# Optimization experiments

Hardware: AMD Instinct MI355X
Metric: run time of the kernel (lower is better)

Reference implementation:

```python
import jax, jax.numpy as jnp
import numpy as np

N_NODES = 10000
N_EDGES = 160000
F_DIM = 64
H = 4


def setup_inputs() -> dict:
    key = jax.random.key(0)
    ks = jax.random.split(key, 10)
    s = 1.0 / np.sqrt(F_DIM)  # xavier-ish scale
    return {
        "x": jax.random.normal(ks[0], (N_NODES, F_DIM), jnp.float32),
        "edge_index": jax.random.randint(ks[1], (2, N_EDGES), 0, N_NODES),
        "edge_vec": jax.random.normal(ks[2], (N_EDGES, 3), jnp.float32),
        "edge_len": jax.random.uniform(ks[3], (N_EDGES,), jnp.float32, 0.1, 5.0),
        "w_proj_W": jax.random.normal(ks[4], (H, F_DIM, F_DIM), jnp.float32) * s,
        "radial_W": jax.random.normal(ks[5], (H, F_DIM, F_DIM), jnp.float32) * s,
        "tangential_W": jax.random.normal(ks[6], (H, F_DIM, F_DIM), jnp.float32) * s,
        "radial_score": jax.random.normal(ks[7], (H, F_DIM), jnp.float32) * s,
        "tangential_score": jax.random.normal(ks[8], (H, F_DIM), jnp.float32) * s,
        "radial_distance_log_scale": jnp.zeros((), jnp.float32),
        "radial_temp_bias": jnp.zeros((H,), jnp.float32),
        "radial_temp_weight": jnp.zeros((H,), jnp.float32),
        "w_out_W": jax.random.normal(ks[9], (F_DIM, F_DIM), jnp.float32) * s,
    }


def _segment_softmax(logits, receiver, num_nodes):
    # logits: [E, H]; softmax over all edges sharing the same receiver.
    # Equivalent to the original's degree-bucketed per-group softmax.
    m = jax.ops.segment_max(logits, receiver, num_segments=num_nodes)  # [N, H]
    a = jnp.exp(logits - m[receiver])
    d = jax.ops.segment_sum(a, receiver, num_segments=num_nodes)       # [N, H]
    return a / d[receiver]


def reference(x, edge_index, edge_vec, edge_len, w_proj_W, radial_W, tangential_W,
              radial_score, tangential_score, radial_distance_log_scale,
              radial_temp_bias, radial_temp_weight, w_out_W):
    sender, receiver = edge_index[0], edge_index[1]
    n = x.shape[0]

    # Per-head bias-free linear projections (o3.Linear on scalar irreps).
    energy = jnp.einsum('nf,hfg->hng', x, w_proj_W)       # [H, N, F]
    radial = jnp.einsum('nf,hfg->hng', x, radial_W)       # [H, N, F]
    tang = jnp.einsum('nf,hfg->hng', x, tangential_W)     # [H, N, F]

    e_d = energy[:, sender] - energy[:, receiver]                       # [H, E, F]
    r_d = jnp.transpose(radial[:, sender] - radial[:, receiver], (1, 0, 2))  # [E, H, F]
    t_d = jnp.transpose(tang[:, sender] - tang[:, receiver], (1, 0, 2))      # [E, H, F]

    scale = jax.nn.softplus(radial_distance_log_scale)
    r_log = jnp.einsum('hef,hf->eh', e_d, radial_score) - scale * edge_len[:, None]  # [E, H]
    temp = jax.nn.softplus(radial_temp_bias[None, :] + radial_temp_weight[None, :] * edge_len[:, None])
    r_log = r_log / (temp + 0.0001)
    t_log = jnp.einsum('hef,hf->eh', e_d, tangential_score)                          # [E, H]

    r_alpha = _segment_softmax(r_log, receiver, n)  # [E, H]
    t_alpha = _segment_softmax(t_log, receiver, n)  # [E, H]

    r_msg = jax.ops.segment_sum(r_alpha[:, :, None] * r_d, receiver, num_segments=n)  # [N, H, F]
    t_msg = jax.ops.segment_sum(t_alpha[:, :, None] * t_d, receiver, num_segments=n)  # [N, H, F]

    out = jnp.nan_to_num((r_msg + t_msg).mean(axis=1))  # mean over heads -> [N, F]
    return x + out @ w_out_W
```

## Files before the change

kernel.cpp:

```cpp
#include <hip/hip_runtime.h>
#include <math.h>

#define N_NODES 10000
#define N_EDGES 160000
#define CAP 64

#define NB_SCORE 40
#define NB_BUCKET 625
#define NB_WPP 9
#define NB_D1 (NB_SCORE + NB_BUCKET + NB_WPP)

typedef short bf16x8 __attribute__((ext_vector_type(8)));
typedef float f32x4 __attribute__((ext_vector_type(4)));

__device__ __forceinline__ float bf2f(unsigned short u) {
    return __uint_as_float(((unsigned int)u) << 16);
}
__device__ __forceinline__ unsigned short f2bf(float f) {
    unsigned int x = __float_as_uint(f);
    unsigned int r = (x + 0x7fffu + ((x >> 16) & 1u)) >> 16;
    return (unsigned short)r;
}
__device__ __forceinline__ float softplus_f(float x) {
    return fmaxf(x, 0.f) + log1pf(expf(-fabsf(x)));
}

__global__ void __launch_bounds__(256) k_prep(const float* __restrict__ x,
                                              const float* __restrict__ wproj,
                                              const float* __restrict__ wrad,
                                              const float* __restrict__ wtan,
                                              const float* __restrict__ rsc,
                                              const float* __restrict__ tsc,
                                              const float* __restrict__ wout,
                                              const int* __restrict__ ei,
                                              const float* __restrict__ el,
                                              float* __restrict__ rs,
                                              float* __restrict__ ts,
                                              int* __restrict__ cur,
                                              int2* __restrict__ sbuf,
                                              unsigned short* __restrict__ wppT) {
    __shared__ __align__(16) float smem[8192];
    int b = blockIdx.x;
    int t = threadIdx.x;

    if (b < NB_SCORE) {
        float* vrl = smem;
        float* vtl = smem + 256;
        {
            int h = t >> 6, f = t & 63;
            const float* wrow = wproj + h * 4096 + f * 64;
            const float* rsp = rsc + h * 64;
            const float* tsp = tsc + h * 64;
            float ar = 0.f, at = 0.f;
            for (int g = 0; g < 64; ++g) {
                float w = wrow[g];
                ar += w * rsp[g];
                at += w * tsp[g];
            }
            vrl[t] = ar;
            vtl[t] = at;
        }
        __syncthreads();
        int n = b * 256 + t;
        if (n >= N_NODES) return;
        const float4* xr = (const float4*)(x + n * 64);
        float accr[4] = {0.f, 0.f, 0.f, 0.f};
        float acct[4] = {0.f, 0.f, 0.f, 0.f};
        for (int i = 0; i < 16; ++i) {
            float4 xv = xr[i];
#pragma unroll
            for (int h = 0; h < 4; ++h) {
                float4 a = ((const float4*)vrl)[h * 16 + i];
                accr[h] += xv.x * a.x + xv.y * a.y + xv.z * a.z + xv.w * a.w;
                float4 bb = ((const float4*)vtl)[h * 16 + i];
                acct[h] += xv.x * bb.x + xv.y * bb.y + xv.z * bb.z + xv.w * bb.w;
            }
        }
        ((float4*)rs)[n] = make_float4(accr[0], accr[1], accr[2], accr[3]);
        ((float4*)ts)[n] = make_float4(acct[0], acct[1], acct[2], acct[3]);
    } else if (b < NB_SCORE + NB_BUCKET) {
        int e = (b - NB_SCORE) * 256 + t;
        if (e >= N_EDGES) return;
        int s = ei[e];
        int r = ei[N_EDGES + e];
        float len = el[e];
        int pos = atomicAdd(&cur[r], 1);
        if (pos < CAP) sbuf[r * CAP + pos] = make_int2(s, __float_as_int(len));
    } else {
        int k = b - NB_SCORE - NB_BUCKET;
        float* wo = smem;
        float* am = smem + 4096;
        for (int i = 0; i < 16; ++i) wo[t + 256 * i] = wout[t + 256 * i];
        if (k < 8) {
            const float* M = (k < 4) ? (wrad + k * 4096) : (wtan + (k - 4) * 4096);
            for (int i = 0; i < 16; ++i) am[t + 256 * i] = M[t + 256 * i];
        } else {
            for (int i = 0; i < 16; ++i) {
                int e = t + 256 * i;
                float s = 0.f;
#pragma unroll
                for (int h = 0; h < 4; ++h) s += wrad[h * 4096 + e] + wtan[h * 4096 + e];
                am[e] = -s;
            }
        }
        __syncthreads();
        int c = t & 63;
        int fg = t >> 6;
        for (int j = 0; j < 16; ++j) {
            int f = fg * 16 + j;
            float acc = 0.f;
            for (int g = 0; g < 64; ++g) acc += am[f * 64 + g] * wo[g * 64 + c];
            wppT[c * 576 + k * 64 + f] = f2bf(acc * 0.25f);
        }
    }
}

__global__ void __launch_bounds__(1024, 8) k_node(const int* __restrict__ cur,
                                                  const int2* __restrict__ sbuf,
                                                  const float* __restrict__ rs,
                                                  const float* __restrict__ ts,
                                                  const float* __restrict__ rdls,
                                                  const float* __restrict__ tb,
                                                  const float* __restrict__ tw,
                                                  const float* __restrict__ x,
                                                  const unsigned short* __restrict__ wppT,
                                                  float* __restrict__ out) {
    __shared__ __align__(16) unsigned short accL[16 * 584];
    __shared__ __align__(16) float aldsb[16][CAP * 8];
    __shared__ int sldsb[16][CAP];
    int t = threadIdx.x;
    int wid = t >> 6, lane = t & 63;
    int blk = blockIdx.x;

    float scale = softplus_f(rdls[0]);
    float tb0 = tb[0], tb1 = tb[1], tb2 = tb[2], tb3 = tb[3];
    float tw0 = tw[0], tw1 = tw[1], tw2 = tw[2], tw3 = tw[3];
    float* alds = aldsb[wid];
    int*   slds = sldsb[wid];

    int n = blk * 16 + wid;
    int deg = min(cur[n], CAP);

    float4 rsr = ((const float4*)rs)[n];
    float4 tsr = ((const float4*)ts)[n];

    const float NEG = -3.402823466e38f;
    float rl0 = NEG, rl1 = NEG, rl2 = NEG, rl3 = NEG;
    float tl0 = NEG, tl1 = NEG, tl2 = NEG, tl3 = NEG;
    int s_e = 0;
    if (lane < deg) {
        int2 sl = sbuf[n * CAP + lane];
        s_e = sl.x;
        float len = __int_as_float(sl.y);
        float4 rss = ((const float4*)rs)[s_e];
        float4 tss = ((const float4*)ts)[s_e];
        float sl0 = scale * len;
        float i0 = 1.f / (softplus_f(tb0 + tw0 * len) + 1e-4f);
        float i1 = 1.f / (softplus_f(tb1 + tw1 * len) + 1e-4f);
        float i2 = 1.f / (softplus_f(tb2 + tw2 * len) + 1e-4f);
        float i3 = 1.f / (softplus_f(tb3 + tw3 * len) + 1e-4f);
        rl0 = ((rss.x - rsr.x) - sl0) * i0;
        rl1 = ((rss.y - rsr.y) - sl0) * i1;
        rl2 = ((rss.z - rsr.z) - sl0) * i2;
        rl3 = ((rss.w - rsr.w) - sl0) * i3;
        tl0 = tss.x - tsr.x;
        tl1 = tss.y - tsr.y;
        tl2 = tss.z - tsr.z;
        tl3 = tss.w - tsr.w;
    }
    float mr0 = rl0, mr1 = rl1, mr2 = rl2, mr3 = rl3;
    float mt0 = tl0, mt1 = tl1, mt2 = tl2, mt3 = tl3;
#pragma unroll
    for (int d = 32; d >= 1; d >>= 1) {
        mr0 = fmaxf(mr0, __shfl_xor(mr0, d)); mr1 = fmaxf(mr1, __shfl_xor(mr1, d));
        mr2 = fmaxf(mr2, __shfl_xor(mr2, d)); mr3 = fmaxf(mr3, __shfl_xor(mr3, d));
        mt0 = fmaxf(mt0, __shfl_xor(mt0, d)); mt1 = fmaxf(mt1, __shfl_xor(mt1, d));
        mt2 = fmaxf(mt2, __shfl_xor(mt2, d)); mt3 = fmaxf(mt3, __shfl_xor(mt3, d));
    }
    float er0 = 0.f, er1 = 0.f, er2 = 0.f, er3 = 0.f;
    float et0 = 0.f, et1 = 0.f, et2 = 0.f, et3 = 0.f;
    if (lane < deg) {
        er0 = expf(rl0 - mr0); er1 = expf(rl1 - mr1);
        er2 = expf(rl2 - mr2); er3 = expf(rl3 - mr3);
        et0 = expf(tl0 - mt0); et1 = expf(tl1 - mt1);
        et2 = expf(tl2 - mt2); et3 = expf(tl3 - mt3);
    }
    float sr0 = er0, sr1 = er1, sr2 = er2, sr3 = er3;
    float st0 = et0, st1 = et1, st2 = et2, st3 = et3;
#pragma unroll
    for (int d = 32; d >= 1; d >>= 1) {
        sr0 += __shfl_xor(sr0, d); sr1 += __shfl_xor(sr1, d);
        sr2 += __shfl_xor(sr2, d); sr3 += __shfl_xor(sr3, d);
        st0 += __shfl_xor(st0, d); st1 += __shfl_xor(st1, d);
        st2 += __shfl_xor(st2, d); st3 += __shfl_xor(st3, d);
    }
    if (lane < deg) {
        float* ap = alds + lane * 8;
        ((float4*)ap)[0] = make_float4(er0 / sr0, er1 / sr1, er2 / sr2, er3 / sr3);
        ((float4*)ap)[1] = make_float4(et0 / st0, et1 / st1, et2 / st2, et3 / st3);
        slds[lane] = s_e;
    }

    float a0 = 0.f, a1 = 0.f, a2 = 0.f, a3 = 0.f;
    float b0 = 0.f, b1 = 0.f, b2 = 0.f, b3 = 0.f;
    int i = 0;
    for (; i + 4 <= deg; i += 4) {
        int s0 = slds[i], s1 = slds[i + 1], s2 = slds[i + 2], s3 = slds[i + 3];
        float xv0 = x[s0 * 64 + lane];
        float xv1 = x[s1 * 64 + lane];
        float xv2 = x[s2 * 64 + lane];
        float xv3 = x[s3 * 64 + lane];
        float4 ar0 = ((const float4*)(alds + i * 8))[0];
        float4 at0 = ((const float4*)(alds + i * 8))[1];
        float4 ar1 = ((const float4*)(alds + (i + 1) * 8))[0];
        float4 at1 = ((const float4*)(alds + (i + 1) * 8))[1];
        float4 ar2 = ((const float4*)(alds + (i + 2) * 8))[0];
        float4 at2 = ((const float4*)(alds + (i + 2) * 8))[1];
        float4 ar3 = ((const float4*)(alds + (i + 3) * 8))[0];
        float4 at3 = ((const float4*)(alds + (i + 3) * 8))[1];
        a0 += ar0.x * xv0 + ar1.x * xv1 + ar2.x * xv2 + ar3.x * xv3;
        a1 += ar0.y * xv0 + ar1.y * xv1 + ar2.y * xv2 + ar3.y * xv3;
        a2 += ar0.z * xv0 + ar1.z * xv1 + ar2.z * xv2 + ar3.z * xv3;
        a3 += ar0.w * xv0 + ar1.w * xv1 + ar2.w * xv2 + ar3.w * xv3;
        b0 += at0.x * xv0 + at1.x * xv1 + at2.x * xv2 + at3.x * xv3;
        b1 += at0.y * xv0 + at1.y * xv1 + at2.y * xv2 + at3.y * xv3;
        b2 += at0.z * xv0 + at1.z * xv1 + at2.z * xv2 + at3.z * xv3;
        b3 += at0.w * xv0 + at1.w * xv1 + at2.w * xv2 + at3.w * xv3;
    }
    for (; i < deg; ++i) {
        int s0 = slds[i];
        float xv0 = x[s0 * 64 + lane];
        float4 ar0 = ((const float4*)(alds + i * 8))[0];
        float4 at0 = ((const float4*)(alds + i * 8))[1];
        a0 += ar0.x * xv0; a1 += ar0.y * xv0; a2 += ar0.z * xv0; a3 += ar0.w * xv0;
        b0 += at0.x * xv0; b1 += at0.y * xv0; b2 += at0.z * xv0; b3 += at0.w * xv0;
    }
    float c8 = (deg > 0) ? x[n * 64 + lane] : 0.f;

    unsigned short* arow = accL + wid * 584;
    arow[0 * 64 + lane] = f2bf(a0);
    arow[1 * 64 + lane] = f2bf(a1);
    arow[2 * 64 + lane] = f2bf(a2);
    arow[3 * 64 + lane] = f2bf(a3);
    arow[4 * 64 + lane] = f2bf(b0);
    arow[5 * 64 + lane] = f2bf(b1);
    arow[6 * 64 + lane] = f2bf(b2);
    arow[7 * 64 + lane] = f2bf(b3);
    arow[8 * 64 + lane] = f2bf(c8);
    __syncthreads();

    if (wid < 4) {
        int c = lane & 15, q = lane >> 4;
        f32x4 dacc = {0.f, 0.f, 0.f, 0.f};
        const unsigned short* bp = wppT + (16 * wid + c) * 576 + q * 8;
        const unsigned short* ap = accL + c * 584 + q * 8;
#pragma unroll
        for (int kc = 0; kc < 18; ++kc) {
            bf16x8 af = *(const bf16x8*)(ap + kc * 32);
            bf16x8 bf = *(const bf16x8*)(bp + kc * 32);
            dacc = __builtin_amdgcn_mfma_f32_16x16x32_bf16(af, bf, dacc, 0, 0, 0);
        }
#pragma unroll
        for (int r = 0; r < 4; ++r) {
            int node = blk * 16 + q * 4 + r;
            int col = 16 * wid + c;
            out[node * 64 + col] = x[node * 64 + col] + dacc[r];
        }
    }
}

extern "C" void kernel_launch(void* const* d_in, const int* in_sizes, int n_in,
                              void* d_out, int out_size, void* d_ws, size_t ws_size,
                              hipStream_t stream) {
    const float* x     = (const float*)d_in[0];
    const int*   ei    = (const int*)d_in[1];
    const float* el    = (const float*)d_in[3];
    const float* wproj = (const float*)d_in[4];
    const float* wrad  = (const float*)d_in[5];
    const float* wtan  = (const float*)d_in[6];
    const float* rsc   = (const float*)d_in[7];
    const float* tsc   = (const float*)d_in[8];
    const float* rdls  = (const float*)d_in[9];
    const float* tb    = (const float*)d_in[10];
    const float* tw    = (const float*)d_in[11];
    const float* wout  = (const float*)d_in[12];
    float* out = (float*)d_out;

    char* w = (char*)d_ws;
    size_t o = 0;
    auto nxt = [&](size_t bytes) -> char* {
        char* p = w + o;
        o += (bytes + 255) & ~(size_t)255;
        return p;
    };
    float* rs = (float*)nxt((size_t)N_NODES * 4 * 4);
    float* ts = (float*)nxt((size_t)N_NODES * 4 * 4);
    int*   cur = (int*)nxt((size_t)N_NODES * 4);
    int2*  sbuf = (int2*)nxt((size_t)N_NODES * CAP * 8);
    unsigned short* wppT = (unsigned short*)nxt((size_t)64 * 576 * 2);

    hipMemsetAsync(cur, 0, (size_t)N_NODES * 4, stream);

    k_prep<<<NB_D1, 256, 0, stream>>>(x, wproj, wrad, wtan, rsc, tsc, wout,
                                      ei, el, rs, ts, cur, sbuf, wppT);
    k_node<<<625, 1024, 0, stream>>>(cur, sbuf, rs, ts, rdls, tb, tw, x, wppT, out);
}
```

Baseline: 127.1 us.

## Fuse memset, prep and node kernels into one persistent kernel with grid barriers

Replaces the memset plus two kernel launches with a single persistent kernel of 512 blocks that zeroes the counters, runs the prep tasks (scores, edge bucketing, weight prefold) on a subset of blocks, and then processes node tiles in a grid-stride loop. A software sense-reversing grid barrier separates the phases, removing launch overhead and inter-kernel gaps. It also interleaves the radial and tangential score arrays into one buffer and switches expf to __expf. The risk is that the grid barrier assumes all 512 blocks of 1024 threads are co-resident; if they are not, the kernel deadlocks. Phase imbalance also means blocks may idle at the barrier.

Measured after the change: 229.7 us. 1.81x slower.

```diff
diff --git a/kernel.cpp b/kernel.cpp
--- a/kernel.cpp
+++ b/kernel.cpp
@@ -4,11 +4,7 @@
 #define N_NODES 10000
 #define N_EDGES 160000
 #define CAP 64
-
-#define NB_SCORE 40
-#define NB_BUCKET 625
-#define NB_WPP 9
-#define NB_D1 (NB_SCORE + NB_BUCKET + NB_WPP)
+#define GRID 512
 
 typedef short bf16x8 __attribute__((ext_vector_type(8)));
 typedef float f32x4 __attribute__((ext_vector_type(4)));
@@ -22,249 +18,277 @@
     return (unsigned short)r;
 }
 __device__ __forceinline__ float softplus_f(float x) {
-    return fmaxf(x, 0.f) + log1pf(expf(-fabsf(x)));
-}
-
-__global__ void __launch_bounds__(256) k_prep(const float* __restrict__ x,
-                                              const float* __restrict__ wproj,
-                                              const float* __restrict__ wrad,
-                                              const float* __restrict__ wtan,
-                                              const float* __restrict__ rsc,
-                                              const float* __restrict__ tsc,
-                                              const float* __restrict__ wout,
-                                              const int* __restrict__ ei,
-                                              const float* __restrict__ el,
-                                              float* __restrict__ rs,
-                                              float* __restrict__ ts,
-                                              int* __restrict__ cur,
-                                              int2* __restrict__ sbuf,
-                                              unsigned short* __restrict__ wppT) {
-    __shared__ __align__(16) float smem[8192];
+    return fmaxf(x, 0.f) + log1pf(__expf(-fabsf(x)));
+}
+
+__device__ unsigned int g_cnt = 0;
+__device__ unsigned int g_sense = 0;
+
+__device__ __forceinline__ void gbar() {
+    __syncthreads();
+    if (threadIdx.x == 0) {
+        unsigned int e = __hip_atomic_load(&g_sense, __ATOMIC_RELAXED, __HIP_MEMORY_SCOPE_AGENT);
+        unsigned int old = __hip_atomic_fetch_add(&g_cnt, 1, __ATOMIC_RELEASE, __HIP_MEMORY_SCOPE_AGENT);
+        if (old == GRID - 1) {
+            __hip_atomic_store(&g_cnt, 0, __ATOMIC_RELAXED, __HIP_MEMORY_SCOPE_AGENT);
+            __hip_atomic_fetch_add(&g_sense, 1, __ATOMIC_RELEASE, __HIP_MEMORY_SCOPE_AGENT);
+        } else {
+            while (__hip_atomic_load(&g_sense, __ATOMIC_RELAXED, __HIP_MEMORY_SCOPE_AGENT) == e)
+                __builtin_amdgcn_s_sleep(2);
+        }
+        __builtin_amdgcn_fence(__ATOMIC_ACQUIRE, "agent");
+    }
+    __syncthreads();
+}
+
+__global__ void __launch_bounds__(1024, 8) k_fused(const float* __restrict__ x,
+                                                   const int* __restrict__ ei,
+                                                   const float* __restrict__ el,
+                                                   const float* __restrict__ wproj,
+                                                   const float* __restrict__ wrad,
+                                                   const float* __restrict__ wtan,
+                                                   const float* __restrict__ rsc,
+                                                   const float* __restrict__ tsc,
+                                                   const float* __restrict__ rdls,
+                                                   const float* __restrict__ tb,
+                                                   const float* __restrict__ tw,
+                                                   const float* __restrict__ wout,
+                                                   float* __restrict__ rts,
+                                                   int* __restrict__ cur,
+                                                   int2* __restrict__ sbuf,
+                                                   unsigned short* __restrict__ wppT,
+                                                   float* __restrict__ out) {
+    __shared__ __align__(16) char smem[55552];
     int b = blockIdx.x;
     int t = threadIdx.x;
-
-    if (b < NB_SCORE) {
-        float* vrl = smem;
-        float* vtl = smem + 256;
-        {
-            int h = t >> 6, f = t & 63;
-            const float* wrow = wproj + h * 4096 + f * 64;
-            const float* rsp = rsc + h * 64;
-            const float* tsp = tsc + h * 64;
-            float ar = 0.f, at = 0.f;
-            for (int g = 0; g < 64; ++g) {
-                float w = wrow[g];
-                ar += w * rsp[g];
-                at += w * tsp[g];
-            }
-            vrl[t] = ar;
-            vtl[t] = at;
-        }
-        __syncthreads();
-        int n = b * 256 + t;
-        if (n >= N_NODES) return;
-        const float4* xr = (const float4*)(x + n * 64);
-        float accr[4] = {0.f, 0.f, 0.f, 0.f};
-        float acct[4] = {0.f, 0.f, 0.f, 0.f};
-        for (int i = 0; i < 16; ++i) {
-            float4 xv = xr[i];
-#pragma unroll
-            for (int h = 0; h < 4; ++h) {
-                float4 a = ((const float4*)vrl)[h * 16 + i];
-                accr[h] += xv.x * a.x + xv.y * a.y + xv.z * a.z + xv.w * a.w;
-                float4 bb = ((const float4*)vtl)[h * 16 + i];
-                acct[h] += xv.x * bb.x + xv.y * bb.y + xv.z * bb.z + xv.w * bb.w;
-            }
-        }
-        ((float4*)rs)[n] = make_float4(accr[0], accr[1], accr[2], accr[3]);
-        ((float4*)ts)[n] = make_float4(acct[0], acct[1], acct[2], acct[3]);
-    } else if (b < NB_SCORE + NB_BUCKET) {
-        int e = (b - NB_SCORE) * 256 + t;
-        if (e >= N_EDGES) return;
-        int s = ei[e];
-        int r = ei[N_EDGES + e];
-        float len = el[e];
-        int pos = atomicAdd(&cur[r], 1);
-        if (pos < CAP) sbuf[r * CAP + pos] = make_int2(s, __float_as_int(len));
-    } else {
-        int k = b - NB_SCORE - NB_BUCKET;
-        float* wo = smem;
-        float* am = smem + 4096;
-        for (int i = 0; i < 16; ++i) wo[t + 256 * i] = wout[t + 256 * i];
-        if (k < 8) {
-            const float* M = (k < 4) ? (wrad + k * 4096) : (wtan + (k - 4) * 4096);
-            for (int i = 0; i < 16; ++i) am[t + 256 * i] = M[t + 256 * i];
+    int wid = t >> 6, lane = t & 63;
+
+    {
+        int idx = b * 1024 + t;
+        if (idx < N_NODES) cur[idx] = 0;
+    }
+    gbar();
+
+    if (b >= 336) {
+        int task = 511 - b;
+        if (task < 10) {
+            float* vrl = (float*)smem;
+            float* vtl = vrl + 256;
+            if (t < 256) {
+                int h = t >> 6, f = t & 63;
+                const float* wrow = wproj + h * 4096 + f * 64;
+                const float* rsp = rsc + h * 64;
+                const float* tsp = tsc + h * 64;
+                float ar = 0.f, at = 0.f;
+                for (int g = 0; g < 64; ++g) {
+                    float w = wrow[g];
+                    ar += w * rsp[g];
+                    at += w * tsp[g];
+                }
+                vrl[t] = ar;
+                vtl[t] = at;
+            }
+            __syncthreads();
+            int n = task * 1024 + t;
+            if (n < N_NODES) {
+                const float4* xr = (const float4*)(x + n * 64);
+                float accr[4] = {0.f, 0.f, 0.f, 0.f};
+                float acct[4] = {0.f, 0.f, 0.f, 0.f};
+                for (int i = 0; i < 16; ++i) {
+                    float4 xv = xr[i];
+#pragma unroll
+                    for (int h = 0; h < 4; ++h) {
+                        float4 a = ((const float4*)vrl)[h * 16 + i];
+                        accr[h] += xv.x * a.x + xv.y * a.y + xv.z * a.z + xv.w * a.w;
+                        float4 bb = ((const float4*)vtl)[h * 16 + i];
+                        acct[h] += xv.x * bb.x + xv.y * bb.y + xv.z * bb.z + xv.w * bb.w;
+                    }
+                }
+                ((float4*)rts)[n * 2]     = make_float4(accr[0], accr[1], accr[2], accr[3]);
+                ((float4*)rts)[n * 2 + 1] = make_float4(acct[0], acct[1], acct[2], acct[3]);
+            }
+        } else if (task < 167) {
+            int e = (task - 10) * 1024 + t;
+            if (e < N_EDGES) {
+                int s = ei[e];
+                int r = ei[N_EDGES + e];
+                float len = el[e];
+                int pos = atomicAdd(&cur[r], 1);
+                if (pos < CAP) sbuf[r * CAP + pos] = make_int2(s, __float_as_int(len));
+            }
         } else {
-            for (int i = 0; i < 16; ++i) {
-                int e = t + 256 * i;
-                float s = 0.f;
-#pragma unroll
-                for (int h = 0; h < 4; ++h) s += wrad[h * 4096 + e] + wtan[h * 4096 + e];
-                am[e] = -s;
-            }
-        }
-        __syncthreads();
-        int c = t & 63;
-        int fg = t >> 6;
-        for (int j = 0; j < 16; ++j) {
-            int f = fg * 16 + j;
-            float acc = 0.f;
-            for (int g = 0; g < 64; ++g) acc += am[f * 64 + g] * wo[g * 64 + c];
-            wppT[c * 576 + k * 64 + f] = f2bf(acc * 0.25f);
+            int k = task - 167;
+            float* wo = (float*)smem;
+            float* am = wo + 4096;
+            for (int i = 0; i < 4; ++i) wo[t + 1024 * i] = wout[t + 1024 * i];
+            if (k < 8) {
+                const float* M = (k < 4) ? (wrad + k * 4096) : (wtan + (k - 4) * 4096);
+                for (int i = 0; i < 4; ++i) am[t + 1024 * i] = M[t + 1024 * i];
+            } else {
+                for (int i = 0; i < 4; ++i) {
+                    int e = t + 1024 * i;
+                    float s = 0.f;
+#pragma unroll
+                    for (int h = 0; h < 4; ++h) s += wrad[h * 4096 + e] + wtan[h * 4096 + e];
+                    am[e] = -s;
+                }
+            }
+            __syncthreads();
+            int c = t & 63;
+            int fg = t >> 6;
+#pragma unroll
+            for (int j = 0; j < 4; ++j) {
+                int f = fg * 4 + j;
+                float acc = 0.f;
+                for (int g = 0; g < 64; ++g) acc += am[f * 64 + g] * wo[g * 64 + c];
+                wppT[c * 576 + k * 64 + f] = f2bf(acc * 0.25f);
+            }
         }
     }
-}
-
-__global__ void __launch_bounds__(1024, 8) k_node(const int* __restrict__ cur,
-                                                  const int2* __restrict__ sbuf,
-                                                  const float* __restrict__ rs,
-                                                  const float* __restrict__ ts,
-                                                  const float* __restrict__ rdls,
-                                                  const float* __restrict__ tb,
-                                                  const float* __restrict__ tw,
-                                                  const float* __restrict__ x,
-                                                  const unsigned short* __restrict__ wppT,
-                                                  float* __restrict__ out) {
-    __shared__ __align__(16) unsigned short accL[16 * 584];
-    __shared__ __align__(16) float aldsb[16][CAP * 8];
-    __shared__ int sldsb[16][CAP];
-    int t = threadIdx.x;
-    int wid = t >> 6, lane = t & 63;
-    int blk = blockIdx.x;
+    gbar();
+
+    float* aldsb = (float*)smem;
+    unsigned short* accL = (unsigned short*)(smem + 32768);
+    int* sldsb = (int*)(smem + 51456);
+    float* alds = aldsb + wid * 512;
+    int*   slds = sldsb + wid * 64;
 
     float scale = softplus_f(rdls[0]);
     float tb0 = tb[0], tb1 = tb[1], tb2 = tb[2], tb3 = tb[3];
     float tw0 = tw[0], tw1 = tw[1], tw2 = tw[2], tw3 = tw[3];
-    float* alds = aldsb[wid];
-    int*   slds = sldsb[wid];
-
-    int n = blk * 16 + wid;
-    int deg = min(cur[n], CAP);
-
-    float4 rsr = ((const float4*)rs)[n];
-    float4 tsr = ((const float4*)ts)[n];
-
-    const float NEG = -3.402823466e38f;
-    float rl0 = NEG, rl1 = NEG, rl2 = NEG, rl3 = NEG;
-    float tl0 = NEG, tl1 = NEG, tl2 = NEG, tl3 = NEG;
-    int s_e = 0;
-    if (lane < deg) {
-        int2 sl = sbuf[n * CAP + lane];
-        s_e = sl.x;
-        float len = __int_as_float(sl.y);
-        float4 rss = ((const float4*)rs)[s_e];
-        float4 tss = ((const float4*)ts)[s_e];
-        float sl0 = scale * len;
-        float i0 = 1.f / (softplus_f(tb0 + tw0 * len) + 1e-4f);
-        float i1 = 1.f / (softplus_f(tb1 + tw1 * len) + 1e-4f);
-        float i2 = 1.f / (softplus_f(tb2 + tw2 * len) + 1e-4f);
-        float i3 = 1.f / (softplus_f(tb3 + tw3 * len) + 1e-4f);
-        rl0 = ((rss.x - rsr.x) - sl0) * i0;
-        rl1 = ((rss.y - rsr.y) - sl0) * i1;
-        rl2 = ((rss.z - rsr.z) - sl0) * i2;
-        rl3 = ((rss.w - rsr.w) - sl0) * i3;
-        tl0 = tss.x - tsr.x;
-        tl1 = tss.y - tsr.y;
-        tl2 = tss.z - tsr.z;
-        tl3 = tss.w - tsr.w;
-    }
-    float mr0 = rl0, mr1 = rl1, mr2 = rl2, mr3 = rl3;
-    float mt0 = tl0, mt1 = tl1, mt2 = tl2, mt3 = tl3;
-#pragma unroll
-    for (int d = 32; d >= 1; d >>= 1) {
-        mr0 = fmaxf(mr0, __shfl_xor(mr0, d)); mr1 = fmaxf(mr1, __shfl_xor(mr1, d));
-        mr2 = fmaxf(mr2, __shfl_xor(mr2, d)); mr3 = fmaxf(mr3, __shfl_xor(mr3, d));
-        mt0 = fmaxf(mt0, __shfl_xor(mt0, d)); mt1 = fmaxf(mt1, __shfl_xor(mt1, d));
-        mt2 = fmaxf(mt2, __shfl_xor(mt2, d)); mt3 = fmaxf(mt3, __shfl_xor(mt3, d));
-    }
-    float er0 = 0.f, er1 = 0.f, er2 = 0.f, er3 = 0.f;
-    float et0 = 0.f, et1 = 0.f, et2 = 0.f, et3 = 0.f;
-    if (lane < deg) {
-        er0 = expf(rl0 - mr0); er1 = expf(rl1 - mr1);
-        er2 = expf(rl2 - mr2); er3 = expf(rl3 - mr3);
-        et0 = expf(tl0 - mt0); et1 = expf(tl1 - mt1);
-        et2 = expf(tl2 - mt2); et3 = expf(tl3 - mt3);
-    }
-    float sr0 = er0, sr1 = er1, sr2 = er2, sr3 = er3;
-    float st0 = et0, st1 = et1, st2 = et2, st3 = et3;
-#pragma unroll
-    for (int d = 32; d >= 1; d >>= 1) {
-        sr0 += __shfl_xor(sr0, d); sr1 += __shfl_xor(sr1, d);
-        sr2 += __shfl_xor(sr2, d); sr3 += __shfl_xor(sr3, d);
-        st0 += __shfl_xor(st0, d); st1 += __shfl_xor(st1, d);
-        st2 += __shfl_xor(st2, d); st3 += __shfl_xor(st3, d);
-    }
-    if (lane < deg) {
-        float* ap = alds + lane * 8;
-        ((float4*)ap)[0] = make_float4(er0 / sr0, er1 / sr1, er2 / sr2, er3 / sr3);
-        ((float4*)ap)[1] = make_float4(et0 / st0, et1 / st1, et2 / st2, et3 / st3);
-        slds[lane] = s_e;
-    }
-
-    float a0 = 0.f, a1 = 0.f, a2 = 0.f, a3 = 0.f;
-    float b0 = 0.f, b1 = 0.f, b2 = 0.f, b3 = 0.f;
-    int i = 0;
-    for (; i + 4 <= deg; i += 4) {
-        int s0 = slds[i], s1 = slds[i + 1], s2 = slds[i + 2], s3 = slds[i + 3];
-        float xv0 = x[s0 * 64 + lane];
-        float xv1 = x[s1 * 64 + lane];
-        float xv2 = x[s2 * 64 + lane];
-        float xv3 = x[s3 * 64 + lane];
-        float4 ar0 = ((const float4*)(alds + i * 8))[0];
-        float4 at0 = ((const float4*)(alds + i * 8))[1];
-        float4 ar1 = ((const float4*)(alds + (i + 1) * 8))[0];
-        float4 at1 = ((const float4*)(alds + (i + 1) * 8))[1];
-        float4 ar2 = ((const float4*)(alds + (i + 2) * 8))[0];
-        float4 at2 = ((const float4*)(alds + (i + 2) * 8))[1];
-        float4 ar3 = ((const float4*)(alds + (i + 3) * 8))[0];
-        float4 at3 = ((const float4*)(alds + (i + 3) * 8))[1];
-        a0 += ar0.x * xv0 + ar1.x * xv1 + ar2.x * xv2 + ar3.x * xv3;
-        a1 += ar0.y * xv0 + ar1.y * xv1 + ar2.y * xv2 + ar3.y * xv3;
-        a2 += ar0.z * xv0 + ar1.z * xv1 + ar2.z * xv2 + ar3.z * xv3;
-        a3 += ar0.w * xv0 + ar1.w * xv1 + ar2.w * xv2 + ar3.w * xv3;
-        b0 += at0.x * xv0 + at1.x * xv1 + at2.x * xv2 + at3.x * xv3;
-        b1 += at0.y * xv0 + at1.y * xv1 + at2.y * xv2 + at3.y * xv3;
-        b2 += at0.z * xv0 + at1.z * xv1 + at2.z * xv2 + at3.z * xv3;
-        b3 += at0.w * xv0 + at1.w * xv1 + at2.w * xv2 + at3.w * xv3;
-    }
-    for (; i < deg; ++i) {
-        int s0 = slds[i];
-        float xv0 = x[s0 * 64 + lane];
-        float4 ar0 = ((const float4*)(alds + i * 8))[0];
-        float4 at0 = ((const float4*)(alds + i * 8))[1];
-        a0 += ar0.x * xv0; a1 += ar0.y * xv0; a2 += ar0.z * xv0; a3 += ar0.w * xv0;
-        b0 += at0.x * xv0; b1 += at0.y * xv0; b2 += at0.z * xv0; b3 += at0.w * xv0;
-    }
-    float c8 = (deg > 0) ? x[n * 64 + lane] : 0.f;
-
-    unsigned short* arow = accL + wid * 584;
-    arow[0 * 64 + lane] = f2bf(a0);
-    arow[1 * 64 + lane] = f2bf(a1);
-    arow[2 * 64 + lane] = f2bf(a2);
-    arow[3 * 64 + lane] = f2bf(a3);
-    arow[4 * 64 + lane] = f2bf(b0);
-    arow[5 * 64 + lane] = f2bf(b1);
-    arow[6 * 64 + lane] = f2bf(b2);
-    arow[7 * 64 + lane] = f2bf(b3);
-    arow[8 * 64 + lane] = f2bf(c8);
-    __syncthreads();
-
-    if (wid < 4) {
-        int c = lane & 15, q = lane >> 4;
-        f32x4 dacc = {0.f, 0.f, 0.f, 0.f};
-        const unsigned short* bp = wppT + (16 * wid + c) * 576 + q * 8;
-        const unsigned short* ap = accL + c * 584 + q * 8;
-#pragma unroll
-        for (int kc = 0; kc < 18; ++kc) {
-            bf16x8 af = *(const bf16x8*)(ap + kc * 32);
-            bf16x8 bf = *(const bf16x8*)(bp + kc * 32);
-            dacc = __builtin_amdgcn_mfma_f32_16x16x32_bf16(af, bf, dacc, 0, 0, 0);
-        }
-#pragma unroll
-        for (int r = 0; r < 4; ++r) {
-            int node = blk * 16 + q * 4 + r;
-            int col = 16 * wid + c;
-            out[node * 64 + col] = x[node * 64 + col] + dacc[r];
+
+    for (int r = 0; r < 2; ++r) {
+        int bb = b + r * GRID;
+        if (bb >= 625) break;
+        if (r == 1) __syncthreads();
+        int n = bb * 16 + wid;
+        int deg = min(cur[n], CAP);
+
+        float4 rsr = ((const float4*)rts)[n * 2];
+        float4 tsr = ((const float4*)rts)[n * 2 + 1];
+
+        const float NEG = -3.402823466e38f;
+        float rl0 = NEG, rl1 = NEG, rl2 = NEG, rl3 = NEG;
+        float tl0 = NEG, tl1 = NEG, tl2 = NEG, tl3 = NEG;
+        int s_e = 0;
+        if (lane < deg) {
+            int2 sl = sbuf[n * CAP + lane];
+            s_e = sl.x;
+            float len = __int_as_float(sl.y);
+            float4 rss = ((const float4*)rts)[s_e * 2];
+            float4 tss = ((const float4*)rts)[s_e * 2 + 1];
+            float sl0 = scale * len;
+            float i0 = 1.f / (softplus_f(tb0 + tw0 * len) + 1e-4f);
+            float i1 = 1.f / (softplus_f(tb1 + tw1 * len) + 1e-4f);
+            float i2 = 1.f / (softplus_f(tb2 + tw2 * len) + 1e-4f);
+            float i3 = 1.f / (softplus_f(tb3 + tw3 * len) + 1e-4f);
+            rl0 = ((rss.x - rsr.x) - sl0) * i0;
+            rl1 = ((rss.y - rsr.y) - sl0) * i1;
+            rl2 = ((rss.z - rsr.z) - sl0) * i2;
+            rl3 = ((rss.w - rsr.w) - sl0) * i3;
+            tl0 = tss.x - tsr.x;
+            tl1 = tss.y - tsr.y;
+            tl2 = tss.z - tsr.z;
+            tl3 = tss.w - tsr.w;
+        }
+        float mr0 = rl0, mr1 = rl1, mr2 = rl2, mr3 = rl3;
+        float mt0 = tl0, mt1 = tl1, mt2 = tl2, mt3 = tl3;
+#pragma unroll
+        for (int d = 32; d >= 1; d >>= 1) {
+            mr0 = fmaxf(mr0, __shfl_xor(mr0, d)); mr1 = fmaxf(mr1, __shfl_xor(mr1, d));
+            mr2 = fmaxf(mr2, __shfl_xor(mr2, d)); mr3 = fmaxf(mr3, __shfl_xor(mr3, d));
+            mt0 = fmaxf(mt0, __shfl_xor(mt0, d)); mt1 = fmaxf(mt1, __shfl_xor(mt1, d));
+            mt2 = fmaxf(mt2, __shfl_xor(mt2, d)); mt3 = fmaxf(mt3, __shfl_xor(mt3, d));
+        }
+        float er0 = 0.f, er1 = 0.f, er2 = 0.f, er3 = 0.f;
+        float et0 = 0.f, et1 = 0.f, et2 = 0.f, et3 = 0.f;
+        if (lane < deg) {
+            er0 = __expf(rl0 - mr0); er1 = __expf(rl1 - mr1);
+            er2 = __expf(rl2 - mr2); er3 = __expf(rl3 - mr3);
+            et0 = __expf(tl0 - mt0); et1 = __expf(tl1 - mt1);
+            et2 = __expf(tl2 - mt2); et3 = __expf(tl3 - mt3);
+        }
+        float sr0 = er0, sr1 = er1, sr2 = er2, sr3 = er3;
+        float st0 = et0, st1 = et1, st2 = et2, st3 = et3;
+#pragma unroll
+        for (int d = 32; d >= 1; d >>= 1) {
+            sr0 += __shfl_xor(sr0, d); sr1 += __shfl_xor(sr1, d);
+            sr2 += __shfl_xor(sr2, d); sr3 += __shfl_xor(sr3, d);
+            st0 += __shfl_xor(st0, d); st1 += __shfl_xor(st1, d);
+            st2 += __shfl_xor(st2, d); st3 += __shfl_xor(st3, d);
+        }
+        if (lane < deg) {
+            float* ap = alds + lane * 8;
+            ((float4*)ap)[0] = make_float4(er0 / sr0, er1 / sr1, er2 / sr2, er3 / sr3);
+            ((float4*)ap)[1] = make_float4(et0 / st0, et1 / st1, et2 / st2, et3 / st3);
+            slds[lane] = s_e;
+        }
+
+        float a0 = 0.f, a1 = 0.f, a2 = 0.f, a3 = 0.f;
+        float b0 = 0.f, b1 = 0.f, b2 = 0.f, b3 = 0.f;
+        int i = 0;
+        for (; i + 4 <= deg; i += 4) {
+            int s0 = slds[i], s1 = slds[i + 1], s2 = slds[i + 2], s3 = slds[i + 3];
+            float xv0 = x[s0 * 64 + lane];
+            float xv1 = x[s1 * 64 + lane];
+            float xv2 = x[s2 * 64 + lane];
+            float xv3 = x[s3 * 64 + lane];
+            float4 ar0 = ((const float4*)(alds + i * 8))[0];
+            float4 at0 = ((const float4*)(alds + i * 8))[1];
+            float4 ar1 = ((const float4*)(alds + (i + 1) * 8))[0];
+            float4 at1 = ((const float4*)(alds + (i + 1) * 8))[1];
+            float4 ar2 = ((const float4*)(alds + (i + 2) * 8))[0];
+            float4 at2 = ((const float4*)(alds + (i + 2) * 8))[1];
+            float4 ar3 = ((const float4*)(alds + (i + 3) * 8))[0];
+            float4 at3 = ((const float4*)(alds + (i + 3) * 8))[1];
+            a0 += ar0.x * xv0 + ar1.x * xv1 + ar2.x * xv2 + ar3.x * xv3;
+            a1 += ar0.y * xv0 + ar1.y * xv1 + ar2.y * xv2 + ar3.y * xv3;
+            a2 += ar0.z * xv0 + ar1.z * xv1 + ar2.z * xv2 + ar3.z * xv3;
+            a3 += ar0.w * xv0 + ar1.w * xv1 + ar2.w * xv2 + ar3.w * xv3;
+            b0 += at0.x * xv0 + at1.x * xv1 + at2.x * xv2 + at3.x * xv3;
+            b1 += at0.y * xv0 + at1.y * xv1 + at2.y * xv2 + at3.y * xv3;
+            b2 += at0.z * xv0 + at1.z * xv1 + at2.z * xv2 + at3.z * xv3;
+            b3 += at0.w * xv0 + at1.w * xv1 + at2.w * xv2 + at3.w * xv3;
+        }
+        for (; i < deg; ++i) {
+            int s0 = slds[i];
+            float xv0 = x[s0 * 64 + lane];
+            float4 ar0 = ((const float4*)(alds + i * 8))[0];
+            float4 at0 = ((const float4*)(alds + i * 8))[1];
+            a0 += ar0.x * xv0; a1 += ar0.y * xv0; a2 += ar0.z * xv0; a3 += ar0.w * xv0;
+            b0 += at0.x * xv0; b1 += at0.y * xv0; b2 += at0.z * xv0; b3 += at0.w * xv0;
+        }
+        float c8 = (deg > 0) ? x[n * 64 + lane] : 0.f;
+
+        unsigned short* arow = accL + wid * 584;
+        arow[0 * 64 + lane] = f2bf(a0);
+        arow[1 * 64 + lane] = f2bf(a1);
+        arow[2 * 64 + lane] = f2bf(a2);
+        arow[3 * 64 + lane] = f2bf(a3);
+        arow[4 * 64 + lane] = f2bf(b0);
+        arow[5 * 64 + lane] = f2bf(b1);
+        arow[6 * 64 + lane] = f2bf(b2);
+        arow[7 * 64 + lane] = f2bf(b3);
+        arow[8 * 64 + lane] = f2bf(c8);
+        __syncthreads();
+
+        if (wid < 4) {
+            int c = lane & 15, q = lane >> 4;
+            f32x4 dacc = {0.f, 0.f, 0.f, 0.f};
+            const unsigned short* bp = wppT + (16 * wid + c) * 576 + q * 8;
+            const unsigned short* ap = accL + c * 584 + q * 8;
+#pragma unroll
+            for (int kc = 0; kc < 18; ++kc) {
+                bf16x8 af = *(const bf16x8*)(ap + kc * 32);
+                bf16x8 bf = *(const bf16x8*)(bp + kc * 32);
+                dacc = __builtin_amdgcn_mfma_f32_16x16x32_bf16(af, bf, dacc, 0, 0, 0);
+            }
+#pragma unroll
+            for (int rr = 0; rr < 4; ++rr) {
+                int node = bb * 16 + q * 4 + rr;
+                int col = 16 * wid + c;
+                out[node * 64 + col] = x[node * 64 + col] + dacc[rr];
+            }
         }
     }
 }
@@ -293,15 +317,12 @@
         o += (bytes + 255) & ~(size_t)255;
         return p;
     };
-    float* rs = (float*)nxt((size_t)N_NODES * 4 * 4);
-    float* ts = (float*)nxt((size_t)N_NODES * 4 * 4);
+    float* rts = (float*)nxt((size_t)N_NODES * 8 * 4);
     int*   cur = (int*)nxt((size_t)N_NODES * 4);
     int2*  sbuf = (int2*)nxt((size_t)N_NODES * CAP * 8);
     unsigned short* wppT = (unsigned short*)nxt((size_t)64 * 576 * 2);
 
-    hipMemsetAsync(cur, 0, (size_t)N_NODES * 4, stream);
-
-    k_prep<<<NB_D1, 256, 0, stream>>>(x, wproj, wrad, wtan, rsc, tsc, wout,
-                                      ei, el, rs, ts, cur, sbuf, wppT);
-    k_node<<<625, 1024, 0, stream>>>(cur, sbuf, rs, ts, rdls, tb, tw, x, wppT, out);
-}
+    k_fused<<<GRID, 1024, 0, stream>>>(x, ei, el, wproj, wrad, wtan, rsc, tsc,
+                                       rdls, tb, tw, wout,
+                                       rts, cur, sbuf, wppT, out);
+}
```

## Drop memset via self-resetting device counters, interleave score arrays, use fast exp

Applied to the files above, without the earlier changes.

The per-receiver edge counters move into a static device array that the node kernel resets to zero after reading, so the separate hipMemsetAsync launch is no longer needed. The radial and tangential per-node scores are interleaved into one buffer, so each gather touches one 32-byte region instead of two separate arrays. expf is replaced by __expf in the softmax and softplus. The risk is that correctness now relies on state carried between calls: the counters start at zero only because the previous invocation cleared them, so an aborted run leaves them dirty. __expf is also less accurate.

After: 122.4 us. 3.7% less time.

```diff
diff --git a/kernel.cpp b/kernel.cpp
--- a/kernel.cpp
+++ b/kernel.cpp
@@ -13,6 +13,8 @@
 typedef short bf16x8 __attribute__((ext_vector_type(8)));
 typedef float f32x4 __attribute__((ext_vector_type(4)));
 
+__device__ int g_cur[N_NODES];
+
 __device__ __forceinline__ float bf2f(unsigned short u) {
     return __uint_as_float(((unsigned int)u) << 16);
 }
@@ -22,7 +24,7 @@
     return (unsigned short)r;
 }
 __device__ __forceinline__ float softplus_f(float x) {
-    return fmaxf(x, 0.f) + log1pf(expf(-fabsf(x)));
+    return fmaxf(x, 0.f) + log1pf(__expf(-fabsf(x)));
 }
 
 __global__ void __launch_bounds__(256) k_prep(const float* __restrict__ x,
@@ -34,9 +36,7 @@
                                               const float* __restrict__ wout,
                                               const int* __restrict__ ei,
                                               const float* __restrict__ el,
-                                              float* __restrict__ rs,
-                                              float* __restrict__ ts,
-                                              int* __restrict__ cur,
+                                              float* __restrict__ rts,
                                               int2* __restrict__ sbuf,
                                               unsigned short* __restrict__ wppT) {
     __shared__ __align__(16) float smem[8192];
@@ -76,15 +76,15 @@
                 acct[h] += xv.x * bb.x + xv.y * bb.y + xv.z * bb.z + xv.w * bb.w;
             }
         }
-        ((float4*)rs)[n] = make_float4(accr[0], accr[1], accr[2], accr[3]);
-        ((float4*)ts)[n] = make_float4(acct[0], acct[1], acct[2], acct[3]);
+        ((float4*)rts)[n * 2]     = make_float4(accr[0], accr[1], accr[2], accr[3]);
+        ((float4*)rts)[n * 2 + 1] = make_float4(acct[0], acct[1], acct[2], acct[3]);
     } else if (b < NB_SCORE + NB_BUCKET) {
         int e = (b - NB_SCORE) * 256 + t;
         if (e >= N_EDGES) return;
         int s = ei[e];
         int r = ei[N_EDGES + e];
         float len = el[e];
-        int pos = atomicAdd(&cur[r], 1);
+        int pos = atomicAdd(&g_cur[r], 1);
         if (pos < CAP) sbuf[r * CAP + pos] = make_int2(s, __float_as_int(len));
     } else {
         int k = b - NB_SCORE - NB_BUCKET;
@@ -115,10 +115,8 @@
     }
 }
 
-__global__ void __launch_bounds__(1024, 8) k_node(const int* __restrict__ cur,
-                                                  const int2* __restrict__ sbuf,
-                                                  const float* __restrict__ rs,
-                                                  const float* __restrict__ ts,
+__global__ void __launch_bounds__(1024, 8) k_node(const int2* __restrict__ sbuf,
+                                                  const float* __restrict__ rts,
                                                   const float* __restrict__ rdls,
                                                   const float* __restrict__ tb,
                                                   const float* __restrict__ tw,
@@ -139,10 +137,11 @@
     int*   slds = sldsb[wid];
 
     int n = blk * 16 + wid;
-    int deg = min(cur[n], CAP);
-
-    float4 rsr = ((const float4*)rs)[n];
-    float4 tsr = ((const float4*)ts)[n];
+    int deg = min(g_cur[n], CAP);
+    if (lane == 0) g_cur[n] = 0;
+
+    float4 rsr = ((const float4*)rts)[n * 2];
+    float4 tsr = ((const float4*)rts)[n * 2 + 1];
 
     const float NEG = -3.402823466e38f;
     float rl0 = NEG, rl1 = NEG, rl2 = NEG, rl3 = NEG;
@@ -152,8 +151,8 @@
         int2 sl = sbuf[n * CAP + lane];
         s_e = sl.x;
         float len = __int_as_float(sl.y);
-        float4 rss = ((const float4*)rs)[s_e];
-        float4 tss = ((const float4*)ts)[s_e];
+        float4 rss = ((const float4*)rts)[s_e * 2];
+        float4 tss = ((const float4*)rts)[s_e * 2 + 1];
         float sl0 = scale * len;
         float i0 = 1.f / (softplus_f(tb0 + tw0 * len) + 1e-4f);
         float i1 = 1.f / (softplus_f(tb1 + tw1 * len) + 1e-4f);
@@ -180,10 +179,10 @@
     float er0 = 0.f, er1 = 0.f, er2 = 0.f, er3 = 0.f;
     float et0 = 0.f, et1 = 0.f, et2 = 0.f, et3 = 0.f;
     if (lane < deg) {
-        er0 = expf(rl0 - mr0); er1 = expf(rl1 - mr1);
-        er2 = expf(rl2 - mr2); er3 = expf(rl3 - mr3);
-        et0 = expf(tl0 - mt0); et1 = expf(tl1 - mt1);
-        et2 = expf(tl2 - mt2); et3 = expf(tl3 - mt3);
+        er0 = __expf(rl0 - mr0); er1 = __expf(rl1 - mr1);
+        er2 = __expf(rl2 - mr2); er3 = __expf(rl3 - mr3);
+        et0 = __expf(tl0 - mt0); et1 = __expf(tl1 - mt1);
+        et2 = __expf(tl2 - mt2); et3 = __expf(tl3 - mt3);
     }
     float sr0 = er0, sr1 = er1, sr2 = er2, sr3 = er3;
     float st0 = et0, st1 = et1, st2 = et2, st3 = et3;
@@ -293,15 +292,11 @@
         o += (bytes + 255) & ~(size_t)255;
         return p;
     };
-    float* rs = (float*)nxt((size_t)N_NODES * 4 * 4);
-    float* ts = (float*)nxt((size_t)N_NODES * 4 * 4);
-    int*   cur = (int*)nxt((size_t)N_NODES * 4);
+    float* rts = (float*)nxt((size_t)N_NODES * 8 * 4);
     int2*  sbuf = (int2*)nxt((size_t)N_NODES * CAP * 8);
     unsigned short* wppT = (unsigned short*)nxt((size_t)64 * 576 * 2);
 
-    hipMemsetAsync(cur, 0, (size_t)N_NODES * 4, stream);
-
     k_prep<<<NB_D1, 256, 0, stream>>>(x, wproj, wrad, wtan, rsc, tsc, wout,
-                                      ei, el, rs, ts, cur, sbuf, wppT);
-    k_node<<<625, 1024, 0, stream>>>(cur, sbuf, rs, ts, rdls, tb, tw, x, wppT, out);
-}
+                                      ei, el, rts, sbuf, wppT);
+    k_node<<<625, 1024, 0, stream>>>(sbuf, rts, rdls, tb, tw, x, wppT, out);
+}
```
